# Kernel tuning notes

Measured on AMD Instinct MI355X. Metric: run time of the kernel, lower is better.

## Reference

```python
import jax, jax.numpy as jnp
import numpy as np

NUM_HEADS = 16
HEAD_SIZE = 64
D_MODEL = NUM_HEADS * HEAD_SIZE  # 1024


def setup_inputs() -> dict:
    key = jax.random.key(0)
    k_in, k_ctx, k_q, k_k, k_v, k_o, k_b = jax.random.split(key, 7)
    B, Sq, Skv, D = 4, 2048, 2048, D_MODEL
    inputs = jax.random.normal(k_in, (B, Sq, D), dtype=jnp.float32)
    context = jax.random.normal(k_ctx, (B, Skv, D), dtype=jnp.float32)
    s = 0.02
    Wq = jax.random.normal(k_q, (D, D), dtype=jnp.float32) * s
    Wk = jax.random.normal(k_k, (D, D), dtype=jnp.float32) * s
    Wv = jax.random.normal(k_v, (D, D), dtype=jnp.float32) * s
    Wo = jax.random.normal(k_o, (D, D), dtype=jnp.float32) * s
    bo = jnp.zeros((D,), dtype=jnp.float32)
    return {"inputs": inputs, "context": context, "Wq": Wq, "Wk": Wk,
            "Wv": Wv, "Wo": Wo, "bo": bo}


def reference(inputs, context, Wq, Wk, Wv, Wo, bo):
    # inputs: [B, Sq, D]; context: [B, Skv, D]
    B, Sq, _ = inputs.shape
    H, Dh = NUM_HEADS, HEAD_SIZE
    scale = Dh ** -0.5
    q = (inputs @ Wq).reshape(B, Sq, H, Dh)          # [B,Sq,H,Dh]
    k = (context @ Wk).reshape(B, -1, H, Dh)          # [B,Skv,H,Dh]
    v = (context @ Wv).reshape(B, -1, H, Dh)
    # The chunked online-softmax recurrence in the source is exactly softmax attention.
    scores = jnp.einsum('bqhd,bkhd->bhqk', q, k) * scale
    probs = jax.nn.softmax(scores, axis=-1)
    attn = jnp.einsum('bhqk,bkhd->bqhd', probs, v)    # [B,Sq,H,Dh]
    out = attn.reshape(B, Sq, H * Dh)
    return out @ Wo + bo
```

## Files before the change

kernel.cpp:

```cpp
#include <hip/hip_runtime.h>
#include <hip/hip_bf16.h>


#define D_MODEL 1024
#define NHEAD   16
#define DHEAD   64
#define BATCH   4
#define SEQ     2048
#define MROWS   (BATCH * SEQ)
#define WP      ((size_t)D_MODEL * D_MODEL)

typedef unsigned short u16;
typedef __attribute__((ext_vector_type(8))) _Float16       f16x8;
typedef __attribute__((ext_vector_type(2))) _Float16       f16x2;
typedef __attribute__((ext_vector_type(4))) float          f32x4;
typedef __attribute__((ext_vector_type(8))) unsigned short u16x8;
typedef __attribute__((ext_vector_type(4))) unsigned short u16x4;

__device__ __forceinline__ u16 f2h(float x) {
    union { _Float16 h; u16 u; } cv;
    cv.h = (_Float16)x;
    return cv.u;
}

__device__ __forceinline__ unsigned pkrtz(float a, float b) {
    unsigned r;
    asm("v_cvt_pkrtz_f16_f32 %0, %1, %2" : "=v"(r) : "v"(a), "v"(b));
    return r;
}

__device__ __forceinline__ f32x4 mfma16h(f16x8 a, f16x8 b, f32x4 c) {
    return __builtin_amdgcn_mfma_f32_16x16x32_f16(a, b, c, 0, 0, 0);
}

__device__ __forceinline__ float exp2fast(float x) {
    float r;
    asm("v_exp_f32 %0, %1" : "=v"(r) : "v"(x));
    return r;
}

__device__ __forceinline__ void glds16(const void* g, void* l) {
    __builtin_amdgcn_global_load_lds(
        (const __attribute__((address_space(1))) void*)g,
        (__attribute__((address_space(3))) void*)l, 16, 0, 0);
}

__global__ __launch_bounds__(256) void prep(const float* __restrict__ ctx,
                                            const float* __restrict__ inp,
                                            u16* __restrict__ ctx16,
                                            u16* __restrict__ in16,
                                            const float* __restrict__ W0,
                                            const float* __restrict__ W1,
                                            const float* __restrict__ W2,
                                            const float* __restrict__ W3,
                                            u16* __restrict__ wt, float qscale) {
    __shared__ u16 th[64 * 64];
    const int id = blockIdx.x;
    const int t = threadIdx.x;

    if (id < 4096) {
        const size_t i = ((size_t)id * 256 + t) * 8;
        {
            float4 v0 = *(const float4*)(ctx + i);
            float4 v1 = *(const float4*)(ctx + i + 4);
            u16x8 h;
            h[0] = f2h(v0.x); h[1] = f2h(v0.y); h[2] = f2h(v0.z); h[3] = f2h(v0.w);
            h[4] = f2h(v1.x); h[5] = f2h(v1.y); h[6] = f2h(v1.z); h[7] = f2h(v1.w);
            *(u16x8*)(ctx16 + i) = h;
        }
        {
            float4 v0 = *(const float4*)(inp + i);
            float4 v1 = *(const float4*)(inp + i + 4);
            u16x8 h;
            h[0] = f2h(v0.x); h[1] = f2h(v0.y); h[2] = f2h(v0.z); h[3] = f2h(v0.w);
            h[4] = f2h(v1.x); h[5] = f2h(v1.y); h[6] = f2h(v1.z); h[7] = f2h(v1.w);
            *(u16x8*)(in16 + i) = h;
        }
        return;
    }

    const int id2 = id - 4096;
    const int z = id2 >> 8;
    const int rem = id2 & 255;
    const float* W = (z == 0) ? W0 : (z == 1) ? W1 : (z == 2) ? W2 : W3;
    const float scale = (z == 2) ? qscale : 1.0f;
    u16* T = wt + (size_t)z * WP;
    const int k0 = (rem & 15) * 64, n0 = (rem >> 4) * 64;

#pragma unroll
    for (int rep = 0; rep < 4; ++rep) {
        int kr = (t >> 4) + 16 * rep;
        int nc = (t & 15) * 4;
        float4 v = *(const float4*)(W + (size_t)(k0 + kr) * D_MODEL + n0 + nc);
#pragma unroll
        for (int u = 0; u < 4; ++u) {
            int n = nc + u;
            th[n * 64 + (kr ^ (8 * ((n >> 3) & 7)))] = f2h(((const float*)&v)[u] * scale);
        }
    }
    __syncthreads();
#pragma unroll
    for (int rep = 0; rep < 2; ++rep) {
        int n = (t >> 3) + 32 * rep;
        int kb = (t & 7) * 8;
        int a = n * 64 + (kb ^ (8 * ((n >> 3) & 7)));
        *(u16x8*)(T + (size_t)(n0 + n) * D_MODEL + k0 + kb) = *(const u16x8*)&th[a];
    }
}

__global__ __launch_bounds__(256) void gemm_proj(const u16* __restrict__ Actx,
                                                 const u16* __restrict__ Ainp,
                                                 const u16* __restrict__ Bh,
                                                 u16* __restrict__ Kf,
                                                 u16* __restrict__ Vimg,
                                                 u16* __restrict__ Qf) {
    const int K = 1024;
    __shared__ u16 sA[128 * 32];
    __shared__ u16 sB[128 * 32];

    const int t = threadIdx.x;
    const int w = t >> 6, l = t & 63, g = l >> 4, lr = l & 15;
    const int wrow = (w >> 1) * 64, wcol = (w & 1) * 64;

    const int bid = blockIdx.x;
    const int vg = bid >> 9;
    const int inner = bid & 511;
    const int wgs = (inner & 7) * 64 + (inner >> 3);
    const int bm = wgs >> 3, bn8 = wgs & 7;
    const int bn = vg * 8 + bn8;

    const u16* A16 = (vg < 2) ? Actx : Ainp;

    f32x4 acc[4][4];
#pragma unroll
    for (int i = 0; i < 4; ++i)
#pragma unroll
        for (int j = 0; j < 4; ++j) acc[i][j] = (f32x4){0.f, 0.f, 0.f, 0.f};

    const int srow = t >> 2;
    const int scg  = (t & 3) * 8;

    for (int k0 = 0; k0 < K; k0 += 32) {
#pragma unroll
        for (int rep = 0; rep < 2; ++rep) {
            const int row  = srow + 64 * rep;
            const int lofs = row * 32 + scg;
            glds16(A16 + (size_t)(bm * 128 + row) * K + k0 + scg, &sA[lofs]);
            glds16(Bh  + (size_t)(bn * 128 + row) * K + k0 + scg, &sB[lofs]);
        }
        __syncthreads();

        f16x8 a[4], b[4];
#pragma unroll
        for (int f = 0; f < 4; ++f) {
            a[f] = *(const f16x8*)&sA[(wrow + f * 16 + lr) * 32 + 8 * g];
            b[f] = *(const f16x8*)&sB[(wcol + f * 16 + lr) * 32 + 8 * g];
        }
        __builtin_amdgcn_s_setprio(1);
#pragma unroll
        for (int fi = 0; fi < 4; ++fi)
#pragma unroll
            for (int fj = 0; fj < 4; ++fj)
                acc[fi][fj] = mfma16h(a[fi], b[fj], acc[fi][fj]);
        __builtin_amdgcn_s_setprio(0);
        __syncthreads();
    }

    if (vg == 0) {
#pragma unroll
        for (int fj = 0; fj < 4; ++fj) {
            const int colg = bn8 * 128 + wcol + fj * 16 + lr;
#pragma unroll
            for (int fi = 0; fi < 4; ++fi) {
                const int rowb = bm * 128 + wrow + fi * 16 + 4 * g;
#pragma unroll
                for (int j = 0; j < 4; ++j)
                    Kf[(size_t)(rowb + j) * D_MODEL + colg] = f2h(acc[fi][fj][j]);
            }
        }
    } else if (vg == 1) {
        const int rowb0 = bm * 128 + wrow;
        const int bidx = rowb0 >> 11;
        const int tile = (rowb0 & 2047) >> 6;
#pragma unroll
        for (int fj = 0; fj < 4; ++fj) {
            const int vcol = bn8 * 128 + wcol + fj * 16 + lr;
            const int vh = vcol >> 6, vd = vcol & 63;
            const size_t tbase = ((size_t)((bidx * NHEAD + vh) * 32) + tile) * 4096;
            const int dsw = vd & 7;
#pragma unroll
            for (int fi = 0; fi < 4; ++fi) {
                const int qp = g | ((fi >> 1) << 2);
                const int i0 = (fi & 1) << 2;
                const int q  = qp ^ dsw;
                u16x4 hv;
#pragma unroll
                for (int j = 0; j < 4; ++j) hv[j] = f2h(acc[fi][fj][j]);
                *(u16x4*)(Vimg + tbase + vd * 64 + 8 * q + i0) = hv;
            }
        }
    } else {
#pragma unroll
        for (int fj = 0; fj < 4; ++fj) {
            const int colg = bn8 * 128 + wcol + fj * 16 + lr;
#pragma unroll
            for (int fi = 0; fi < 4; ++fi) {
                const int rowb = bm * 128 + wrow + fi * 16 + 4 * g;
#pragma unroll
                for (int j = 0; j < 4; ++j)
                    Qf[(size_t)(rowb + j) * D_MODEL + colg] = f2h(acc[fi][fj][j]);
            }
        }
    }
}

__global__ __launch_bounds__(256) void gemm_out(const u16* __restrict__ A16,
                                                const u16* __restrict__ Bh,
                                                const float* __restrict__ bias,
                                                float* __restrict__ Cf) {
    const int K = 1024, N = 1024;
    __shared__ u16 sA[64 * 32];
    __shared__ u16 sB[128 * 32];

    const int t = threadIdx.x;
    const int w = t >> 6, l = t & 63, g = l >> 4, lr = l & 15;
    const int wrow = (w >> 1) * 32, wcol = (w & 1) * 64;

    const int bid = blockIdx.x;
    const int wg = (bid & 7) * 128 + (bid >> 3);
    const int bm = wg & 127, bn = wg >> 7;

    f32x4 acc[2][4];
#pragma unroll
    for (int i = 0; i < 2; ++i)
#pragma unroll
        for (int j = 0; j < 4; ++j) acc[i][j] = (f32x4){0.f, 0.f, 0.f, 0.f};

    const int srow = t >> 2;
    const int scg  = (t & 3) * 8;

    for (int k0 = 0; k0 < K; k0 += 32) {
        glds16(A16 + (size_t)(bm * 64 + srow) * K + k0 + scg, &sA[srow * 32 + scg]);
#pragma unroll
        for (int rep = 0; rep < 2; ++rep) {
            const int row = srow + 64 * rep;
            glds16(Bh + (size_t)(bn * 128 + row) * K + k0 + scg, &sB[row * 32 + scg]);
        }
        __syncthreads();

        f16x8 a[2], b[4];
#pragma unroll
        for (int f = 0; f < 2; ++f)
            a[f] = *(const f16x8*)&sA[(wrow + f * 16 + lr) * 32 + 8 * g];
#pragma unroll
        for (int f = 0; f < 4; ++f)
            b[f] = *(const f16x8*)&sB[(wcol + f * 16 + lr) * 32 + 8 * g];
        __builtin_amdgcn_s_setprio(1);
#pragma unroll
        for (int fi = 0; fi < 2; ++fi)
#pragma unroll
            for (int fj = 0; fj < 4; ++fj)
                acc[fi][fj] = mfma16h(a[fi], b[fj], acc[fi][fj]);
        __builtin_amdgcn_s_setprio(0);
        __syncthreads();
    }

#pragma unroll
    for (int fj = 0; fj < 4; ++fj) {
        const int colg = bn * 128 + wcol + fj * 16 + lr;
        const float bv = bias[colg];
#pragma unroll
        for (int fi = 0; fi < 2; ++fi) {
            const int rowb = bm * 64 + wrow + fi * 16 + 4 * g;
#pragma unroll
            for (int j = 0; j < 4; ++j)
                Cf[(size_t)(rowb + j) * N + colg] = acc[fi][fj][j] + bv;
        }
    }
}

__global__ __launch_bounds__(512, 4) void attn_mfma10(const u16* __restrict__ Qf,
                                                      const u16* __restrict__ Kf,
                                                      const u16* __restrict__ Vimg,
                                                      u16* __restrict__ Af16) {
    const int bid = blockIdx.x;
    const int wg = (bid & 7) * 64 + (bid >> 3);
    const int qt = wg & 7;
    const int hb = wg >> 3;
    const int h = hb & 15, b = hb >> 4;

    const int t = threadIdx.x, w = t >> 6, l = t & 63, g = l >> 4, lr = l & 15;

    __shared__ u16 Ks[2][4096];
    __shared__ u16 Vs[4][4096];

    f16x8 qf[2][2];
#pragma unroll
    for (int qg = 0; qg < 2; ++qg) {
        const size_t qb = (size_t)(b * SEQ + qt * 256 + w * 32 + qg * 16 + lr) * D_MODEL + h * DHEAD;
#pragma unroll
        for (int c = 0; c < 2; ++c)
            qf[qg][c] = *(const f16x8*)(Qf + qb + 32 * c + 8 * g);
    }

    f32x4 o[2][4];
#pragma unroll
    for (int qg = 0; qg < 2; ++qg)
#pragma unroll
        for (int c = 0; c < 4; ++c) o[qg][c] = (f32x4){0.f, 0.f, 0.f, 0.f};
    float lsum[2] = {0.f, 0.f};

    const u16* Kh = Kf + (size_t)(b * SEQ) * D_MODEL + h * DHEAD;
    const size_t vtb = (size_t)((b * NHEAD + h) * 32) * 4096;

    const int kr_ = t >> 3, kd0 = (t & 7) * 8;
    const int ksrc  = kd0 ^ ((kr_ & 7) << 3);
    const int klofs = t * 8;
    const int kkey  = (lr & 7) << 3;

    const f16x2 ones2 = {(_Float16)1.0f, (_Float16)1.0f};

    auto stage = [&](int tile) {
        glds16(Kh + (size_t)((tile << 6) + kr_) * D_MODEL + ksrc, &Ks[tile & 1][klofs]);
        glds16(Vimg + vtb + (size_t)tile * 4096 + (size_t)t * 8, &Vs[tile & 3][klofs]);
    };

    auto qk = [&](const u16* Kbuf, f32x4 (&s)[2][4]) {
#pragma unroll
        for (int qg = 0; qg < 2; ++qg)
#pragma unroll
            for (int rt = 0; rt < 4; ++rt) s[qg][rt] = (f32x4){-4.f, -4.f, -4.f, -4.f};
        __builtin_amdgcn_s_setprio(1);
#pragma unroll
        for (int rt = 0; rt < 4; ++rt) {
            const int rb = (16 * rt + lr) * 64;
#pragma unroll
            for (int c = 0; c < 2; ++c) {
                f16x8 k8 = *(const f16x8*)&Kbuf[rb + ((8 * g + 32 * c) ^ kkey)];
#pragma unroll
                for (int qg = 0; qg < 2; ++qg)
                    s[qg][rt] = mfma16h(k8, qf[qg][c], s[qg][rt]);
            }
        }
        __builtin_amdgcn_s_setprio(0);
    };

    auto smpv = [&](f32x4 (&s)[2][4], const u16* Vbuf) {
#pragma unroll
        for (int qg = 0; qg < 2; ++qg) {
#pragma unroll
            for (int rt = 0; rt < 4; ++rt)
#pragma unroll
                for (int j = 0; j < 4; ++j)
                    s[qg][rt][j] = exp2fast(s[qg][rt][j]);

            float rs = 0.f;
            f16x8 pbq[2];
#pragma unroll
            for (int ks = 0; ks < 2; ++ks) {
                union { unsigned w_[4]; f16x8 v; } pk;
#pragma unroll
                for (int pr = 0; pr < 4; ++pr) {
                    const int rt = 2 * ks + (pr >> 1);
                    const int j0 = (pr & 1) * 2;
                    const unsigned pw = pkrtz(s[qg][rt][j0], s[qg][rt][j0 + 1]);
                    pk.w_[pr] = pw;
                    union { unsigned w_; f16x2 h2; } cv;
                    cv.w_ = pw;
                    rs = __builtin_amdgcn_fdot2(cv.h2, ones2, rs, false);
                }
                pbq[ks] = pk.v;
            }
            lsum[qg] += rs;

            __builtin_amdgcn_s_setprio(1);
#pragma unroll
            for (int ks = 0; ks < 2; ++ks)
#pragma unroll
                for (int c = 0; c < 4; ++c) {
                    const int dv = 16 * c + lr;
                    f16x8 v8 = *(const f16x8*)&Vbuf[dv * 64 + ((8 * g + 32 * ks) ^ ((dv & 7) << 3))];
                    o[qg][c] = mfma16h(v8, pbq[ks], o[qg][c]);
                }
            __builtin_amdgcn_s_setprio(0);
        }
    };

    f32x4 sA[2][4], sB[2][4];

    stage(0);
    __syncthreads();
    stage(1);
    qk(Ks[0], sA);
    __syncthreads();

    for (int oo = 0; oo < 15; ++oo) {
        const int i1 = 2 * oo + 1, i2 = 2 * oo + 2;
        stage(i1 + 1);
        qk(Ks[1], sB);
        smpv(sA, Vs[(i1 - 1) & 3]);
        __syncthreads();
        stage(i2 + 1);
        qk(Ks[0], sA);
        smpv(sB, Vs[(i2 - 1) & 3]);
        __syncthreads();
    }

    qk(Ks[1], sB);
    smpv(sA, Vs[2]);
    smpv(sB, Vs[3]);

#pragma unroll
    for (int qg = 0; qg < 2; ++qg) {
        lsum[qg] += __shfl_xor(lsum[qg], 16);
        lsum[qg] += __shfl_xor(lsum[qg], 32);
        const float inv = 1.f / lsum[qg];
        u16* op = Af16 + (size_t)(b * SEQ + qt * 256 + w * 32 + qg * 16 + lr) * D_MODEL + h * DHEAD;
#pragma unroll
        for (int c = 0; c < 4; ++c) {
            u16x4 hv;
#pragma unroll
            for (int j = 0; j < 4; ++j) hv[j] = f2h(o[qg][c][j] * inv);
            *(u16x4*)(op + 16 * c + 4 * g) = hv;
        }
    }
}

extern "C" void kernel_launch(void* const* d_in, const int* in_sizes, int n_in,
                              void* d_out, int out_size, void* d_ws, size_t ws_size,
                              hipStream_t stream) {
    const float* inputs  = (const float*)d_in[0];
    const float* context = (const float*)d_in[1];
    const float* Wq      = (const float*)d_in[2];
    const float* Wk      = (const float*)d_in[3];
    const float* Wv      = (const float*)d_in[4];
    const float* Wo      = (const float*)d_in[5];
    const float* bo      = (const float*)d_in[6];
    float* out = (float*)d_out;

    const size_t P = (size_t)MROWS * D_MODEL;

    u16* base  = (u16*)d_ws;
    u16* ctx16 = base;
    u16* in16  = base + P;
    u16* kf    = base + 2 * P;
    u16* vimg  = base + 3 * P;
    u16* qf    = base + 4 * P;
    u16* af    = base + 5 * P;
    u16* wt    = base + 6 * P;
    u16* woh   = wt + 3 * WP;

    const float QSCALE = 0.18033688011112042f;

    prep<<<dim3(5120), dim3(256), 0, stream>>>(context, inputs, ctx16, in16,
                                               Wk, Wv, Wq, Wo, wt, QSCALE);

    gemm_proj<<<dim3(1536), dim3(256), 0, stream>>>(ctx16, in16, wt, kf, vimg, qf);

    attn_mfma10<<<dim3(512), dim3(512), 0, stream>>>(qf, kf, vimg, af);

    gemm_out<<<dim3(1024), dim3(256), 0, stream>>>(af, woh, bo, out);
}
```

Baseline: 250.7 us.

## Replace software-pipelined QK/PV attention loop with simple double-buffered loop

The attention kernel previously overlapped the QK MFMA of one KV tile with the softmax/PV of the previous tile, using two score register sets and a 4-deep V buffer. This replaces that with a straightforward per-tile loop: double-buffered K and V in LDS, prefetch of the next tile, then QK, exp and PV on the current tile. It cuts LDS use and register pressure (launch bounds no longer force 4 waves/SIMD occupancy) in exchange for losing the cross-tile MFMA/VALU interleaving.

```diff
diff --git a/kernel.cpp b/kernel.cpp
--- a/kernel.cpp
+++ b/kernel.cpp
@@ -279,20 +279,20 @@
     }
 }
 
-__global__ __launch_bounds__(512, 4) void attn_mfma10(const u16* __restrict__ Qf,
-                                                      const u16* __restrict__ Kf,
-                                                      const u16* __restrict__ Vimg,
-                                                      u16* __restrict__ Af16) {
-    const int bid = blockIdx.x;
-    const int wg = (bid & 7) * 64 + (bid >> 3);
-    const int qt = wg & 7;
-    const int hb = wg >> 3;
+__global__ __launch_bounds__(512) void attn_mfma8(const u16* __restrict__ Qf,
+                                                  const u16* __restrict__ Kf,
+                                                  const u16* __restrict__ Vimg,
+                                                  u16* __restrict__ Af16) {
+    const int bid  = blockIdx.x;
+    const int wgid = (bid & 7) * 64 + (bid >> 3);
+    const int qt = wgid & 7;
+    const int hb = wgid >> 3;
     const int h = hb & 15, b = hb >> 4;
 
     const int t = threadIdx.x, w = t >> 6, l = t & 63, g = l >> 4, lr = l & 15;
 
     __shared__ u16 Ks[2][4096];
-    __shared__ u16 Vs[4][4096];
+    __shared__ u16 Vs[2][4096];
 
     f16x8 qf[2][2];
 #pragma unroll
@@ -320,12 +320,19 @@
 
     const f16x2 ones2 = {(_Float16)1.0f, (_Float16)1.0f};
 
-    auto stage = [&](int tile) {
-        glds16(Kh + (size_t)((tile << 6) + kr_) * D_MODEL + ksrc, &Ks[tile & 1][klofs]);
-        glds16(Vimg + vtb + (size_t)tile * 4096 + (size_t)t * 8, &Vs[tile & 3][klofs]);
+    auto stage = [&](int bb, int kv0) {
+        glds16(Kh + (size_t)(kv0 + kr_) * D_MODEL + ksrc, &Ks[bb][klofs]);
+        glds16(Vimg + vtb + (size_t)(kv0 >> 6) * 4096 + (size_t)t * 8, &Vs[bb][klofs]);
     };
 
-    auto qk = [&](const u16* Kbuf, f32x4 (&s)[2][4]) {
+    stage(0, 0);
+
+    for (int it = 0; it < SEQ / 64; ++it) {
+        const int cb = it & 1;
+        __syncthreads();
+        if (it < SEQ / 64 - 1) stage(cb ^ 1, (it + 1) << 6);
+
+        f32x4 s[2][4];
 #pragma unroll
         for (int qg = 0; qg < 2; ++qg)
 #pragma unroll
@@ -336,16 +343,15 @@
             const int rb = (16 * rt + lr) * 64;
 #pragma unroll
             for (int c = 0; c < 2; ++c) {
-                f16x8 k8 = *(const f16x8*)&Kbuf[rb + ((8 * g + 32 * c) ^ kkey)];
+                const int p = rb + ((8 * g + 32 * c) ^ kkey);
+                f16x8 k8 = *(const f16x8*)&Ks[cb][p];
 #pragma unroll
                 for (int qg = 0; qg < 2; ++qg)
                     s[qg][rt] = mfma16h(k8, qf[qg][c], s[qg][rt]);
             }
         }
         __builtin_amdgcn_s_setprio(0);
-    };
-
-    auto smpv = [&](f32x4 (&s)[2][4], const u16* Vbuf) {
+
 #pragma unroll
         for (int qg = 0; qg < 2; ++qg) {
 #pragma unroll
@@ -379,36 +385,12 @@
 #pragma unroll
                 for (int c = 0; c < 4; ++c) {
                     const int dv = 16 * c + lr;
-                    f16x8 v8 = *(const f16x8*)&Vbuf[dv * 64 + ((8 * g + 32 * ks) ^ ((dv & 7) << 3))];
+                    f16x8 v8 = *(const f16x8*)&Vs[cb][dv * 64 + ((8 * g + 32 * ks) ^ ((dv & 7) << 3))];
                     o[qg][c] = mfma16h(v8, pbq[ks], o[qg][c]);
                 }
             __builtin_amdgcn_s_setprio(0);
         }
-    };
-
-    f32x4 sA[2][4], sB[2][4];
-
-    stage(0);
-    __syncthreads();
-    stage(1);
-    qk(Ks[0], sA);
-    __syncthreads();
-
-    for (int oo = 0; oo < 15; ++oo) {
-        const int i1 = 2 * oo + 1, i2 = 2 * oo + 2;
-        stage(i1 + 1);
-        qk(Ks[1], sB);
-        smpv(sA, Vs[(i1 - 1) & 3]);
-        __syncthreads();
-        stage(i2 + 1);
-        qk(Ks[0], sA);
-        smpv(sB, Vs[(i2 - 1) & 3]);
-        __syncthreads();
-    }
-
-    qk(Ks[1], sB);
-    smpv(sA, Vs[2]);
-    smpv(sB, Vs[3]);
+    }
 
 #pragma unroll
     for (int qg = 0; qg < 2; ++qg) {
@@ -457,7 +439,7 @@
 
     gemm_proj<<<dim3(1536), dim3(256), 0, stream>>>(ctx16, in16, wt, kf, vimg, qf);
 
-    attn_mfma10<<<dim3(512), dim3(512), 0, stream>>>(qf, kf, vimg, af);
+    attn_mfma8<<<dim3(512), dim3(512), 0, stream>>>(qf, kf, vimg, af);
 
     gemm_out<<<dim3(1024), dim3(256), 0, stream>>>(af, woh, bo, out);
 }
```

Result: faster. 228.8 us (-8.7%).
